# Kernel tuning notes

Hardware: AMD Instinct MI355X
Metric: run time of the kernel (lower is better)

## Reference

```python
import jax, jax.numpy as jnp
import numpy as np

EPS = 1e-12  # matches torch F.normalize / CosineSimilarity eps scale (1e-12 / 1e-8; vectors are unit so effect is negligible)


def setup_inputs() -> dict:
    key = jax.random.key(0)
    X = jax.random.normal(key, (64, 1024, 128), dtype=jnp.float32)
    return {"X": X}


def reference(X) -> jnp.ndarray:
    # F.normalize(X, dim=-1)
    Xn = X / jnp.maximum(jnp.linalg.norm(X, axis=-1, keepdims=True), EPS)
    # CosineSimilarity on unit vectors == batched X @ X^T  -> [B, scale, scale]
    S = jnp.einsum("bsd,btd->bst", Xn, Xn)
    # MSE vs ones per batch, averaged over batch == global mean of (S-1)^2
    return jnp.mean((S - 1.0) ** 2)
```

## Files before the change

kernel.cpp:

```cpp
#include <hip/hip_runtime.h>
#include <hip/hip_bf16.h>


#define BATCH 64
#define SEQ   1024
#define DIM   128

typedef short short8  __attribute__((ext_vector_type(8)));
typedef float floatx4 __attribute__((ext_vector_type(4)));

__device__ __forceinline__ unsigned bf16rne(float x) {
    unsigned u = __builtin_bit_cast(unsigned, x);
    return (u + 0x7FFFu + ((u >> 16) & 1u)) >> 16;
}

#define XNT_B  0
#define VP_B   16777216
#define RES_B  (VP_B + 1024 * 256 * 4)
#define CNT_B  (RES_B + 512 * 4)


__global__ __launch_bounds__(256, 4)
void kA_norm_t(const float* __restrict__ X, unsigned* __restrict__ XnT,
               float* __restrict__ vpartA, int* __restrict__ counter) {
    __shared__ __align__(16) float lds[64][140];
    const int t     = threadIdx.x;
    const int wg    = blockIdx.x;
    const int b     = wg & 63, chunk = wg >> 6;
    const int sl    = t >> 2, q = t & 3;
    const int f     = t & 127, sh = t >> 7;
    const int rb    = f >> 4, l15 = f & 15;

    if (wg == 0 && t == 0) *counter = 0;

    const float4* rp = (const float4*)(
        X + ((size_t)(b * SEQ + chunk * 64 + sl) * DIM + q * 32));
    float4 g[8];
#pragma unroll
    for (int k = 0; k < 8; ++k) g[k] = rp[k];

    float ssq = 0.0f;
#pragma unroll
    for (int k = 0; k < 8; ++k)
        ssq += g[k].x * g[k].x + g[k].y * g[k].y +
               g[k].z * g[k].z + g[k].w * g[k].w;
    ssq += __shfl_xor(ssq, 1);
    ssq += __shfl_xor(ssq, 2);
    const float inv = rsqrtf(fmaxf(ssq, 1e-24f));

#pragma unroll
    for (int k = 0; k < 8; ++k) {
        float4 n;
        n.x = g[k].x * inv; n.y = g[k].y * inv;
        n.z = g[k].z * inv; n.w = g[k].w * inv;
        *(float4*)&lds[sl][q * 36 + k * 4] = n;
    }
    __syncthreads();

    const int fcol = (f >> 5) * 36 + (f & 31);
    float vacc = 0.0f;
    float v[32];
#pragma unroll
    for (int j = 0; j < 32; ++j) {
        v[j] = lds[sh * 32 + j][fcol];
        vacc += v[j];
    }
    unsigned pk[16];
#pragma unroll
    for (int p = 0; p < 16; ++p)
        pk[p] = bf16rne(v[2 * p]) | (bf16rne(v[2 * p + 1]) << 16);

    const int kk = chunk * 2 + sh;
    uint4* op = (uint4*)(XnT + (((size_t)((b * 8 + rb) * 32 + kk)) << 8));
#pragma unroll
    for (int k = 0; k < 4; ++k)
        op[k * 16 + l15] = make_uint4(pk[4 * k], pk[4 * k + 1],
                                      pk[4 * k + 2], pk[4 * k + 3]);

    vpartA[(size_t)wg * 256 + t] = vacc;
}

__global__ __launch_bounds__(256, 2)
void kB_gram(const unsigned* __restrict__ XnT, const float* __restrict__ vpartA,
             float* __restrict__ res, int* __restrict__ counter,
             float* __restrict__ out) {
    const int t    = threadIdx.x;
    const int wg   = blockIdx.x;
    const int b    = wg & 63, band = wg >> 6;
    const int lane = t & 63, w = t >> 6;

    const unsigned* Ab  = XnT + (((size_t)((b * 8 + band) * 32)) << 8) + lane * 4;
    const unsigned* B0b = XnT + (((size_t)((b * 8 + 2 * w) * 32)) << 8) + lane * 4;
    const unsigned* B1b = XnT + (((size_t)((b * 8 + 2 * w + 1) * 32)) << 8) + lane * 4;

    floatx4 acc0 = {0.f, 0.f, 0.f, 0.f}, acc1 = {0.f, 0.f, 0.f, 0.f};
#pragma unroll 8
    for (int kk = 0; kk < 32; ++kk) {
        short8 a  = *(const short8*)(Ab  + (kk << 8));
        short8 b0 = *(const short8*)(B0b + (kk << 8));
        short8 b1 = *(const short8*)(B1b + (kk << 8));
        acc0 = __builtin_amdgcn_mfma_f32_16x16x32_bf16(a, b0, acc0, 0, 0, 0);
        acc1 = __builtin_amdgcn_mfma_f32_16x16x32_bf16(a, b1, acc1, 0, 0, 0);
    }

    float s = acc0[0] * acc0[0] + acc0[1] * acc0[1] +
              acc0[2] * acc0[2] + acc0[3] * acc0[3] +
              acc1[0] * acc1[0] + acc1[1] * acc1[1] +
              acc1[2] * acc1[2] + acc1[3] * acc1[3];

    if (band == 0 && t < DIM) {
        float vv = 0.0f;
#pragma unroll
        for (int c = 0; c < 16; ++c) {
            const float* p = vpartA + (size_t)(c * 64 + b) * 256;
            vv += p[t] + p[t + 128];
        }
        s -= 2.0f * vv * vv;
    }

#pragma unroll
    for (int m = 1; m < 64; m <<= 1) s += __shfl_xor(s, m);
    __shared__ float wq[4];
    __shared__ int lastflag;
    if (lane == 0) wq[w] = s;
    __syncthreads();
    if (t == 0) {
        res[wg] = wq[0] + wq[1] + wq[2] + wq[3];
        __threadfence();
        lastflag = (atomicAdd(counter, 1) == 511);
    }
    __syncthreads();
    if (lastflag) {
        __threadfence();
        float s2 = res[t] + res[t + 256];
#pragma unroll
        for (int m = 1; m < 64; m <<= 1) s2 += __shfl_xor(s2, m);
        if ((t & 63) == 0) wq[t >> 6] = s2;
        __syncthreads();
        if (t == 0)
            out[0] = (wq[0] + wq[1] + wq[2] + wq[3]) * (1.0f / 67108864.0f)
                     + 1.0f;
    }
}

extern "C" void kernel_launch(void* const* d_in, const int* in_sizes, int n_in,
                              void* d_out, int out_size, void* d_ws, size_t ws_size,
                              hipStream_t stream) {
    const float* X = (const float*)d_in[0];
    char* ws = (char*)d_ws;
    unsigned* XnT  = (unsigned*)(ws + XNT_B);
    float* vpartA  = (float*)(ws + VP_B);
    float* res     = (float*)(ws + RES_B);
    int*   counter = (int*)(ws + CNT_B);

    kA_norm_t<<<1024, 256, 0, stream>>>(X, XnT, vpartA, counter);
    kB_gram<<<512, 256, 0, stream>>>(XnT, vpartA, res, counter, (float*)d_out);
}
```

Before: 93.14 us.

## Replace atomic last-block reduction with separate final kernel; drop LDS padding

Removes the atomic counter and threadfence-based last-block detection in the gram kernel and moves the final 512-element sum into a third single-block kernel. It also shrinks the LDS row stride in the normalize/transpose kernel from 140 to 132 and drops the padded column mapping. The aim is to cut the per-block atomic and fence cost, with an extra kernel launch as the price. The new LDS layout may bring back bank conflicts on the column reads.

```diff
diff --git a/kernel.cpp b/kernel.cpp
--- a/kernel.cpp
+++ b/kernel.cpp
@@ -17,21 +17,18 @@
 #define XNT_B  0
 #define VP_B   16777216
 #define RES_B  (VP_B + 1024 * 256 * 4)
-#define CNT_B  (RES_B + 512 * 4)
 
 
 __global__ __launch_bounds__(256, 4)
 void kA_norm_t(const float* __restrict__ X, unsigned* __restrict__ XnT,
-               float* __restrict__ vpartA, int* __restrict__ counter) {
-    __shared__ __align__(16) float lds[64][140];
+               float* __restrict__ vpartA) {
+    __shared__ __align__(16) float lds[64][132];
     const int t     = threadIdx.x;
     const int wg    = blockIdx.x;
     const int b     = wg & 63, chunk = wg >> 6;
     const int sl    = t >> 2, q = t & 3;
     const int f     = t & 127, sh = t >> 7;
     const int rb    = f >> 4, l15 = f & 15;
-
-    if (wg == 0 && t == 0) *counter = 0;
 
     const float4* rp = (const float4*)(
         X + ((size_t)(b * SEQ + chunk * 64 + sl) * DIM + q * 32));
@@ -53,16 +50,15 @@
         float4 n;
         n.x = g[k].x * inv; n.y = g[k].y * inv;
         n.z = g[k].z * inv; n.w = g[k].w * inv;
-        *(float4*)&lds[sl][q * 36 + k * 4] = n;
+        *(float4*)&lds[sl][q * 32 + k * 4] = n;
     }
     __syncthreads();
 
-    const int fcol = (f >> 5) * 36 + (f & 31);
     float vacc = 0.0f;
     float v[32];
 #pragma unroll
     for (int j = 0; j < 32; ++j) {
-        v[j] = lds[sh * 32 + j][fcol];
+        v[j] = lds[sh * 32 + j][f];
         vacc += v[j];
     }
     unsigned pk[16];
@@ -82,8 +78,7 @@
 
 __global__ __launch_bounds__(256, 2)
 void kB_gram(const unsigned* __restrict__ XnT, const float* __restrict__ vpartA,
-             float* __restrict__ res, int* __restrict__ counter,
-             float* __restrict__ out) {
+             float* __restrict__ res) {
     const int t    = threadIdx.x;
     const int wg   = blockIdx.x;
     const int b    = wg & 63, band = wg >> 6;
@@ -121,26 +116,22 @@
 #pragma unroll
     for (int m = 1; m < 64; m <<= 1) s += __shfl_xor(s, m);
     __shared__ float wq[4];
-    __shared__ int lastflag;
     if (lane == 0) wq[w] = s;
     __syncthreads();
-    if (t == 0) {
-        res[wg] = wq[0] + wq[1] + wq[2] + wq[3];
-        __threadfence();
-        lastflag = (atomicAdd(counter, 1) == 511);
-    }
+    if (t == 0) res[wg] = wq[0] + wq[1] + wq[2] + wq[3];
+}
+
+__global__ __launch_bounds__(256)
+void kF_final(const float* __restrict__ res, float* __restrict__ out) {
+    const int t = threadIdx.x;
+    float s = res[t] + res[t + 256];
+#pragma unroll
+    for (int m = 1; m < 64; m <<= 1) s += __shfl_xor(s, m);
+    __shared__ float wq[4];
+    if ((t & 63) == 0) wq[t >> 6] = s;
     __syncthreads();
-    if (lastflag) {
-        __threadfence();
-        float s2 = res[t] + res[t + 256];
-#pragma unroll
-        for (int m = 1; m < 64; m <<= 1) s2 += __shfl_xor(s2, m);
-        if ((t & 63) == 0) wq[t >> 6] = s2;
-        __syncthreads();
-        if (t == 0)
-            out[0] = (wq[0] + wq[1] + wq[2] + wq[3]) * (1.0f / 67108864.0f)
-                     + 1.0f;
-    }
+    if (t == 0)
+        out[0] = (wq[0] + wq[1] + wq[2] + wq[3]) * (1.0f / 67108864.0f) + 1.0f;
 }
 
 extern "C" void kernel_launch(void* const* d_in, const int* in_sizes, int n_in,
@@ -151,8 +142,8 @@
     unsigned* XnT  = (unsigned*)(ws + XNT_B);
     float* vpartA  = (float*)(ws + VP_B);
     float* res     = (float*)(ws + RES_B);
-    int*   counter = (int*)(ws + CNT_B);
 
-    kA_norm_t<<<1024, 256, 0, stream>>>(X, XnT, vpartA, counter);
-    kB_gram<<<512, 256, 0, stream>>>(XnT, vpartA, res, counter, (float*)d_out);
+    kA_norm_t<<<1024, 256, 0, stream>>>(X, XnT, vpartA);
+    kB_gram<<<512, 256, 0, stream>>>(XnT, vpartA, res);
+    kF_final<<<1, 256, 0, stream>>>(res, (float*)d_out);
 }
```

Result: faster. 85.90 us (-7.8%).
